# Kernel optimization log

Measured on AMD Instinct MI355X. Metric: run time of the kernel, lower is better.

## Reference

```python
import jax, jax.numpy as jnp
import numpy as np

HD = 64          # head_dim
PX = 32          # patches_x
PY = 32          # patches_y
IW = 512.0       # image_width
IH = 512.0       # image_height
C = 4            # cameras
B = 1
H = 12
S = C * PX * PY  # 4096


def _rope_coeffs(pos, feat_dim):
    nf = feat_dim // 2
    freqs = 100.0 ** (-jnp.arange(nf, dtype=jnp.float32) / nf)  # freq_base=100, freq_scale=1
    ang = pos[:, None].astype(jnp.float32) * freqs[None, :]
    # broadcast shape (1, seqlen, 1, nf)
    return jnp.cos(ang)[None, :, None, :], jnp.sin(ang)[None, :, None, :]


def _rope(x, cs, inverse=False):
    cos, sin = cs
    h = x.shape[-1] // 2
    xi, yi = x[..., :h], x[..., h:]
    if inverse:
        return jnp.concatenate([cos * xi - sin * yi, sin * xi + cos * yi], -1)
    return jnp.concatenate([cos * xi + sin * yi, -sin * xi + cos * yi], -1)


def _proj(x, M):
    # x: (b, s, n, f), M: (b, c, D, D) per-camera projection applied to D-sized sub-blocks
    b, s, n, f = x.shape
    c, D = M.shape[1], M.shape[-1]
    xr = x.reshape(b, c, s // c, n, f // D, D)
    return jnp.einsum('bcij,bcpnkj->bcpnki', M, xr).reshape(b, s, n, f)


def _invert_SE3(T):
    Rinv = jnp.swapaxes(T[..., :3, :3], -1, -2)
    t = -jnp.einsum('...ij,...j->...i', Rinv, T[..., :3, 3])
    top = jnp.concatenate([Rinv, t[..., None]], -1)            # (..., 3, 4)
    bot = jnp.zeros_like(top[..., :1, :]).at[..., 0, 3].set(1.0)
    return jnp.concatenate([top, bot], -2)


def _lift_K(K):
    out = jnp.zeros(K.shape[:-2] + (4, 4), K.dtype)
    return out.at[..., :3, :3].set(K).at[..., 3, 3].set(1.0)


def _invert_K(K):
    out = jnp.zeros_like(K)
    out = out.at[..., 0, 0].set(1.0 / K[..., 0, 0]).at[..., 1, 1].set(1.0 / K[..., 1, 1])
    out = out.at[..., 0, 2].set(-K[..., 0, 2] / K[..., 0, 0]).at[..., 1, 2].set(-K[..., 1, 2] / K[..., 1, 1])
    return out.at[..., 2, 2].set(1.0)


def setup_inputs() -> dict:
    key = jax.random.key(0)
    kq, kk, kv, kr, kt, kf = jax.random.split(key, 6)
    q = jax.random.normal(kq, (B, S, H, HD), dtype=jnp.float32)
    k = jax.random.normal(kk, (B, S, H, HD), dtype=jnp.float32)
    v = jax.random.normal(kv, (B, S, H, HD), dtype=jnp.float32)
    # proper SE(3) viewmats: random rotations (det +1) + translations
    A = jax.random.normal(kr, (B, C, 3, 3), dtype=jnp.float32)
    Q, _ = jnp.linalg.qr(A)
    Q = Q * jnp.sign(jnp.linalg.det(Q))[..., None, None]  # det(sQ)=s^3 det(Q) for 3x3
    t = jax.random.normal(kt, (B, C, 3, 1), dtype=jnp.float32)
    top = jnp.concatenate([Q, t], -1)
    bot = jnp.tile(jnp.array([0.0, 0.0, 0.0, 1.0], jnp.float32)[None, None, None, :], (B, C, 1, 1))
    viewmats = jnp.concatenate([top, bot], -2)
    # realistic pinhole intrinsics
    f = 400.0 + 200.0 * jax.random.uniform(kf, (B, C, 2), dtype=jnp.float32)
    Ks = jnp.zeros((B, C, 3, 3), jnp.float32)
    Ks = Ks.at[..., 0, 0].set(f[..., 0]).at[..., 1, 1].set(f[..., 1])
    Ks = Ks.at[..., 0, 2].set(IW / 2).at[..., 1, 2].set(IH / 2).at[..., 2, 2].set(1.0)
    return {'q': q, 'k': k, 'v': v, 'viewmats': viewmats, 'Ks': Ks}


def reference(q, k, v, viewmats, Ks):
    # normalize intrinsics to [-0.5, 0.5] image coords
    Ksn = jnp.zeros_like(Ks)
    Ksn = Ksn.at[..., 0, 0].set(Ks[..., 0, 0] / IW).at[..., 1, 1].set(Ks[..., 1, 1] / IH)
    Ksn = Ksn.at[..., 0, 2].set(Ks[..., 0, 2] / IW - 0.5).at[..., 1, 2].set(Ks[..., 1, 2] / IH - 0.5)
    Ksn = Ksn.at[..., 2, 2].set(1.0)
    P = jnp.einsum('...ij,...jk->...ik', _lift_K(Ksn), viewmats)         # (B,C,4,4)
    P_T = jnp.swapaxes(P, -1, -2)
    P_inv = jnp.einsum('...ij,...jk->...ik', _invert_SE3(viewmats), _lift_K(_invert_K(Ksn)))
    # 2-D patch positions, tiled over cameras (num_register_tokens=0)
    pos_x = jnp.tile(jnp.arange(PX), (PY * C,))
    pos_y = jnp.tile(jnp.repeat(jnp.arange(PY), PX), (C,))
    cx = _rope_coeffs(pos_x, HD // 4)
    cy = _rope_coeffs(pos_y, HD // 4)
    h2, h4 = HD // 2, HD // 4

    def tq(x):
        return jnp.concatenate([_proj(x[..., :h2], P_T), _rope(x[..., h2:h2 + h4], cx), _rope(x[..., h2 + h4:], cy)], -1)

    def tkv(x):
        return jnp.concatenate([_proj(x[..., :h2], P_inv), _rope(x[..., h2:h2 + h4], cx), _rope(x[..., h2 + h4:], cy)], -1)

    def to(x):
        return jnp.concatenate([_proj(x[..., :h2], P), _rope(x[..., h2:h2 + h4], cx, True), _rope(x[..., h2 + h4:], cy, True)], -1)

    qh, kh, vh = tq(q), tkv(k), tkv(v)
    scale = 1.0 / jnp.sqrt(jnp.float32(HD))
    scores = jnp.einsum('bqhd,bkhd->bhqk', qh, kh) * scale
    w = jax.nn.softmax(scores, axis=-1)
    out = jnp.einsum('bhqk,bkhd->bqhd', w, vh)
    return to(out)
```

## Files before the change

### kernel.cpp

```cpp
#include <hip/hip_runtime.h>
#include <cstdint>

#define SQ 4096
#define NH 12
#define NC 4
#define KVB 64
#define NSPLIT 4
#define NTS (SQ / NSPLIT / KVB)

typedef __attribute__((ext_vector_type(8))) __bf16 bf16x8;
typedef __attribute__((ext_vector_type(8))) short short8;
typedef __attribute__((ext_vector_type(4))) short s16x4;
typedef __attribute__((ext_vector_type(4))) float f32x4;
typedef __attribute__((ext_vector_type(16))) float f32x16;
typedef __attribute__((ext_vector_type(4))) unsigned int u32x4;
typedef __attribute__((ext_vector_type(2))) unsigned int u32x2;

__device__ __forceinline__ unsigned short f2bf(float f) {
  unsigned int u = __float_as_uint(f);
  u += 0x7FFFu + ((u >> 16) & 1u);
  return (unsigned short)(u >> 16);
}
__device__ __forceinline__ float bf2f(unsigned short u) {
  return __uint_as_float(((unsigned int)u) << 16);
}
__device__ __forceinline__ unsigned int cvtpk(float lo, float hi) {
  unsigned int r;
  asm("v_cvt_pk_bf16_f32 %0, %1, %2" : "=v"(r) : "v"(lo), "v"(hi));
  return r;
}

__device__ __constant__ float FRQ[8] = {
    1.0f, 0.5623413251903491f, 0.31622776601683794f, 0.17782794100389229f,
    0.1f, 0.05623413251903491f, 0.031622776601683794f, 0.017782794100389229f};

__device__ __forceinline__ float4 mat4(const float4 M[4], float4 x) {
  float4 y;
  y.x = M[0].x * x.x + M[0].y * x.y + M[0].z * x.z + M[0].w * x.w;
  y.y = M[1].x * x.x + M[1].y * x.y + M[1].z * x.z + M[1].w * x.w;
  y.z = M[2].x * x.x + M[2].y * x.y + M[2].z * x.z + M[2].w * x.w;
  y.w = M[3].x * x.x + M[3].y * x.y + M[3].z * x.z + M[3].w * x.w;
  return y;
}
__device__ __forceinline__ float4 rope4(float4 x, float4 p, float4 c, float4 sn, float sgn) {
  float4 y;
  y.x = c.x * x.x + sgn * sn.x * p.x;
  y.y = c.y * x.y + sgn * sn.y * p.y;
  y.z = c.z * x.z + sgn * sn.z * p.z;
  y.w = c.w * x.w + sgn * sn.w * p.w;
  return y;
}
__device__ __forceinline__ float4 sxor2(float4 x) {
  float4 p;
  p.x = __shfl_xor(x.x, 2); p.y = __shfl_xor(x.y, 2);
  p.z = __shfl_xor(x.z, 2); p.w = __shfl_xor(x.w, 2);
  return p;
}
__device__ __forceinline__ void store_bf4(unsigned short* p, float4 v) {
  s16x4 r;
  r[0] = (short)f2bf(v.x); r[1] = (short)f2bf(v.y);
  r[2] = (short)f2bf(v.z); r[3] = (short)f2bf(v.w);
  *(s16x4*)p = r;
}

__device__ __forceinline__ void build_tables(const float* __restrict__ viewmats,
                                             const float* __restrict__ Ks,
                                             float* __restrict__ mats,
                                             float* __restrict__ ct, float* __restrict__ st) {
  const int t = threadIdx.x;
  if (t < 256) {
    int pos = t >> 3, jf = t & 7;
    float rev = (float)pos * FRQ[jf] * 0.15915494309189535f;
    ct[t] = __builtin_amdgcn_cosf(rev);
    st[t] = __builtin_amdgcn_sinf(rev);
  }
  if (t < NC) {
    const float* V = viewmats + t * 16;
    const float* K = Ks + t * 9;
    float fx = K[0] * (1.0f / 512.0f);
    float fy = K[4] * (1.0f / 512.0f);
    float cx = K[2] * (1.0f / 512.0f) - 0.5f;
    float cy = K[5] * (1.0f / 512.0f) - 0.5f;
    float P[16], PT[16], IV[16], PI[16];
    for (int jj = 0; jj < 4; jj++) {
      P[0 * 4 + jj] = fx * V[0 * 4 + jj] + cx * V[2 * 4 + jj];
      P[1 * 4 + jj] = fy * V[1 * 4 + jj] + cy * V[2 * 4 + jj];
      P[2 * 4 + jj] = V[2 * 4 + jj];
      P[3 * 4 + jj] = V[3 * 4 + jj];
    }
    for (int i = 0; i < 4; i++)
      for (int jj = 0; jj < 4; jj++) PT[i * 4 + jj] = P[jj * 4 + i];
    for (int i = 0; i < 3; i++) {
      for (int jj = 0; jj < 3; jj++) IV[i * 4 + jj] = V[jj * 4 + i];
      IV[i * 4 + 3] = -(V[3] * V[0 * 4 + i] + V[7] * V[1 * 4 + i] + V[11] * V[2 * 4 + i]);
    }
    IV[12] = 0.f; IV[13] = 0.f; IV[14] = 0.f; IV[15] = 1.f;
    float rfx = 1.0f / fx, rfy = 1.0f / fy;
    for (int i = 0; i < 4; i++) {
      PI[i * 4 + 0] = IV[i * 4 + 0] * rfx;
      PI[i * 4 + 1] = IV[i * 4 + 1] * rfy;
      PI[i * 4 + 2] = -cx * rfx * IV[i * 4 + 0] - cy * rfy * IV[i * 4 + 1] + IV[i * 4 + 2];
      PI[i * 4 + 3] = IV[i * 4 + 3];
    }
    for (int ii = 0; ii < 16; ii++) {
      mats[0   + t * 16 + ii] = PT[ii];
      mats[64  + t * 16 + ii] = PI[ii];
      mats[128 + t * 16 + ii] = P[ii];
    }
  }
}

__global__ __launch_bounds__(256) void transform_kernel(
    const float* __restrict__ q, const float* __restrict__ k, const float* __restrict__ v,
    const float* __restrict__ viewmats, const float* __restrict__ Ks,
    unsigned short* __restrict__ qh, unsigned short* __restrict__ kh, unsigned short* __restrict__ vh) {
  __shared__ float TB[192 + 512];
  float* mats = TB;
  float* CT = TB + 192;
  float* ST = TB + 448;
  build_tables(viewmats, Ks, mats, CT, ST);
  __syncthreads();

  const int t = threadIdx.x;
  const int j = t & 15;
  const int rbase = blockIdx.x * 48;
  const int cam = (rbase / NH) >> 10;

  float4 Mq[4], Mk[4];
  if (j < 8) {
    const float4* mq = (const float4*)(mats + cam * 16);
    const float4* mk = (const float4*)(mats + 64 + cam * 16);
#pragma unroll
    for (int i = 0; i < 4; ++i) { Mq[i] = mq[i]; Mk[i] = mk[i]; }
  }

#pragma unroll
  for (int itr = 0; itr < 3; ++itr) {
    const int row = rbase + itr * 16 + (t >> 4);
    const int s = row / NH;
    const int h = row - s * NH;
    const size_t ioff = (size_t)row * 64 + j * 4;
    const size_t ooff = (size_t)h * (SQ * 64) + (size_t)s * 64 + j * 4;
    float4 xq = *(const float4*)(q + ioff);
    float4 xk = *(const float4*)(k + ioff);
    float4 xv = *(const float4*)(v + ioff);
    float4 pq = sxor2(xq), pk = sxor2(xk), pv = sxor2(xv);
    float4 yq, yk, yv;
    if (j < 8) {
      yq = mat4(Mq, xq); yk = mat4(Mk, xk); yv = mat4(Mk, xv);
    } else {
      bool isx = (((j >> 1) & 1) == 0);
      float sgn = isx ? 1.0f : -1.0f;
      int pos = (j < 12) ? (s & 31) : ((s >> 5) & 31);
      int fb = (j & 1) * 4;
      float4 c = *(const float4*)(CT + pos * 8 + fb);
      float4 sn = *(const float4*)(ST + pos * 8 + fb);
      yq = rope4(xq, pq, c, sn, sgn);
      yk = rope4(xk, pk, c, sn, sgn);
      yv = rope4(xv, pv, c, sn, sgn);
    }
    const float SC = 0.1803368801111204f;
    yq.x *= SC; yq.y *= SC; yq.z *= SC; yq.w *= SC;
    store_bf4(qh + ooff, yq);
    store_bf4(kh + ooff, yk);
    store_bf4(vh + ooff, yv);
  }
}

__global__ __launch_bounds__(128, 3) void attn_kernel(const unsigned short* __restrict__ qh,
                                                      const unsigned short* __restrict__ kh,
                                                      const unsigned short* __restrict__ vh,
                                                      unsigned short* __restrict__ opart,
                                                      float* __restrict__ lbuf) {
  __shared__ __align__(16) short Kl[KVB * 64];
  __shared__ __align__(16) short Vl[KVB * 64];
  const int t = threadIdx.x;
  const int lane = t & 63;
  const int w = t >> 6;
  const int hi = lane >> 5;
  const int l31 = lane & 31;
  const int sw7 = l31 & 7;
  const int h = blockIdx.y;
  const int sp = blockIdx.z;
  const int q0 = blockIdx.x * 64 + w * 32;
  const int kbase = sp * (SQ / NSPLIT);
  const size_t hbase = (size_t)h * SQ * 64;

  bf16x8 qf[4];
  {
    const unsigned short* qp = qh + hbase + (size_t)(q0 + l31) * 64 + hi * 8;
#pragma unroll
    for (int ds = 0; ds < 4; ++ds) qf[ds] = *(const bf16x8*)(qp + ds * 16);
  }

  int kr[4], kg[4], kidx[4];
#pragma unroll
  for (int i = 0; i < 4; ++i) {
    int c = t + 128 * i;
    kr[i] = c >> 3;
    kg[i] = c & 7;
    kidx[i] = kr[i] * 64 + ((kg[i] ^ (kr[i] & 7)) << 3);
  }
  const int va = t & 15;
  const int vD0 = (t >> 4) * 8;

  float l = 0.f;
  f32x16 oac0, oac1;
#pragma unroll
  for (int r = 0; r < 16; ++r) { oac0[r] = 0.f; oac1[r] = 0.f; }

  short8 kst[4], vst[4];

  auto issue_loads = [&](int kt) {
#pragma unroll
    for (int i = 0; i < 4; ++i)
      kst[i] = *(const short8*)(kh + hbase + (size_t)(kt + kr[i]) * 64 + kg[i] * 8);
    const unsigned short* vp = vh + hbase + (size_t)(kt + 4 * va) * 64 + vD0;
#pragma unroll
    for (int i = 0; i < 4; ++i) vst[i] = *(const short8*)(vp + i * 64);
  };

  auto write_lds = [&]() {
#pragma unroll
    for (int i = 0; i < 4; ++i) *(short8*)(Kl + kidx[i]) = kst[i];
#pragma unroll
    for (int dd = 0; dd < 8; ++dd) {
      int d = vD0 + dd;
      unsigned int w0 = (unsigned int)(unsigned short)vst[0][dd] |
                        ((unsigned int)(unsigned short)vst[1][dd] << 16);
      unsigned int w1 = (unsigned int)(unsigned short)vst[2][dd] |
                        ((unsigned int)(unsigned short)vst[3][dd] << 16);
      u32x2 pk; pk[0] = w0; pk[1] = w1;
      int idx = d * 64 + ((((va >> 1)) ^ (d & 7)) << 3) + (va & 1) * 4;
      *(u32x2*)(Vl + idx) = pk;
    }
  };

  issue_loads(kbase);
  write_lds();
  __syncthreads();

#define MKFRAG(sv, base, out)                                          \
  {                                                                    \
    unsigned int a0 = cvtpk(sv[base + 0], sv[base + 1]);               \
    unsigned int b0 = cvtpk(sv[base + 4], sv[base + 5]);               \
    asm volatile("v_permlane32_swap_b32 %0, %1" : "+v"(a0), "+v"(b0)); \
    unsigned int a1 = cvtpk(sv[base + 2], sv[base + 3]);               \
    unsigned int b1 = cvtpk(sv[base + 6], sv[base + 7]);               \
    asm volatile("v_permlane32_swap_b32 %0, %1" : "+v"(a1), "+v"(b1)); \
    u32x4 u; u[0] = a0; u[1] = a1; u[2] = b0; u[3] = b1;               \
    out = __builtin_bit_cast(bf16x8, u);                               \
  }

  for (int it = 0; it < NTS; ++it) {
    const bool pf = (it + 1 < NTS);
    if (pf) issue_loads(kbase + (it + 1) * KVB);

    f32x16 s0, s1;
#pragma unroll
    for (int r = 0; r < 16; ++r) { s0[r] = 0.f; s1[r] = 0.f; }
    __builtin_amdgcn_s_setprio(1);
#pragma unroll
    for (int ds = 0; ds < 4; ++ds) {
      bf16x8 k0 = *(const bf16x8*)(Kl + (0 * 32 + l31) * 64 + (((hi + 2 * ds) ^ sw7) << 3));
      bf16x8 k1 = *(const bf16x8*)(Kl + (1 * 32 + l31) * 64 + (((hi + 2 * ds) ^ sw7) << 3));
      s0 = __builtin_amdgcn_mfma_f32_32x32x16_bf16(k0, qf[ds], s0, 0, 0, 0);
      s1 = __builtin_amdgcn_mfma_f32_32x32x16_bf16(k1, qf[ds], s1, 0, 0, 0);
    }
    __builtin_amdgcn_s_setprio(0);

    float rs = 0.f;
#pragma unroll
    for (int r = 0; r < 16; ++r) { s0[r] = __builtin_amdgcn_exp2f(s0[r]); rs += s0[r]; }
#pragma unroll
    for (int r = 0; r < 16; ++r) { s1[r] = __builtin_amdgcn_exp2f(s1[r]); rs += s1[r]; }
    rs += __shfl_xor(rs, 32);
    l += rs;

    bf16x8 pa00, pa01, pa10, pa11;
    MKFRAG(s0, 0, pa00);
    MKFRAG(s0, 8, pa01);
    MKFRAG(s1, 0, pa10);
    MKFRAG(s1, 8, pa11);

    __builtin_amdgcn_s_setprio(1);
#pragma unroll
    for (int db = 0; db < 2; ++db) {
      const int rb = (db * 32 + l31) * 64;
      bf16x8 v00 = *(const bf16x8*)(Vl + rb + (((0 + hi) ^ sw7) << 3));
      bf16x8 v01 = *(const bf16x8*)(Vl + rb + (((2 + hi) ^ sw7) << 3));
      bf16x8 v10 = *(const bf16x8*)(Vl + rb + (((4 + hi) ^ sw7) << 3));
      bf16x8 v11 = *(const bf16x8*)(Vl + rb + (((6 + hi) ^ sw7) << 3));
      if (db == 0) {
        oac0 = __builtin_amdgcn_mfma_f32_32x32x16_bf16(pa00, v00, oac0, 0, 0, 0);
        oac0 = __builtin_amdgcn_mfma_f32_32x32x16_bf16(pa01, v01, oac0, 0, 0, 0);
        oac0 = __builtin_amdgcn_mfma_f32_32x32x16_bf16(pa10, v10, oac0, 0, 0, 0);
        oac0 = __builtin_amdgcn_mfma_f32_32x32x16_bf16(pa11, v11, oac0, 0, 0, 0);
      } else {
        oac1 = __builtin_amdgcn_mfma_f32_32x32x16_bf16(pa00, v00, oac1, 0, 0, 0);
        oac1 = __builtin_amdgcn_mfma_f32_32x32x16_bf16(pa01, v01, oac1, 0, 0, 0);
        oac1 = __builtin_amdgcn_mfma_f32_32x32x16_bf16(pa10, v10, oac1, 0, 0, 0);
        oac1 = __builtin_amdgcn_mfma_f32_32x32x16_bf16(pa11, v11, oac1, 0, 0, 0);
      }
    }
    __builtin_amdgcn_s_setprio(0);
    __syncthreads();
    if (pf) {
      write_lds();
      __syncthreads();
    }
  }

  float linv = 1.0f / l;
  unsigned short* op = opart + (size_t)sp * NH * SQ * 64 + hbase;
#pragma unroll
  for (int r = 0; r < 16; ++r) {
    int qrow = (r & 3) + 8 * (r >> 2) + 4 * hi;
    float lv = __shfl(linv, qrow);
    op[(size_t)(q0 + qrow) * 64 + l31] = f2bf(oac0[r] * lv);
    op[(size_t)(q0 + qrow) * 64 + 32 + l31] = f2bf(oac1[r] * lv);
  }
  if (hi == 0) lbuf[(size_t)sp * NH * SQ + (size_t)h * SQ + q0 + l31] = l;
}

__global__ __launch_bounds__(256) void outtr_kernel(const unsigned short* __restrict__ opart,
                                                    const float* __restrict__ lbuf,
                                                    const float* __restrict__ viewmats,
                                                    const float* __restrict__ Ks,
                                                    float* __restrict__ out) {
  __shared__ float TB[192 + 512];
  float* mats = TB;
  float* CT = TB + 192;
  float* ST = TB + 448;
  build_tables(viewmats, Ks, mats, CT, ST);
  __syncthreads();

  const int t = threadIdx.x;
  const int j = t & 15;
  const int rbase = blockIdx.x * 48;
  const int cam = (rbase / NH) >> 10;

  float4 M[4];
  if (j < 8) {
    const float4* mp = (const float4*)(mats + 128 + cam * 16);
#pragma unroll
    for (int i = 0; i < 4; ++i) M[i] = mp[i];
  }

#pragma unroll
  for (int itr = 0; itr < 3; ++itr) {
    const int row = rbase + itr * 16 + (t >> 4);
    const int s = row / NH;
    const int h = row - s * NH;

    const size_t HSZ = (size_t)NH * SQ * 64;
    float lv[NSPLIT];
    float lsum = 0.f;
#pragma unroll
    for (int sp = 0; sp < NSPLIT; ++sp) {
      lv[sp] = lbuf[(size_t)sp * NH * SQ + (size_t)h * SQ + s];
      lsum += lv[sp];
    }
    float inv = 1.0f / lsum;

    const size_t po = (size_t)h * (SQ * 64) + (size_t)s * 64 + j * 4;
    float4 x = make_float4(0.f, 0.f, 0.f, 0.f);
#pragma unroll
    for (int sp = 0; sp < NSPLIT; ++sp) {
      s16x4 rr = *(const s16x4*)(opart + (size_t)sp * HSZ + po);
      float wv = lv[sp] * inv;
      x.x += bf2f((unsigned short)rr[0]) * wv;
      x.y += bf2f((unsigned short)rr[1]) * wv;
      x.z += bf2f((unsigned short)rr[2]) * wv;
      x.w += bf2f((unsigned short)rr[3]) * wv;
    }

    float4 p = sxor2(x);
    float4 y;
    if (j < 8) {
      y = mat4(M, x);
    } else {
      bool isx = (((j >> 1) & 1) == 0);
      float sgn = isx ? -1.0f : 1.0f;
      int pos = (j < 12) ? (s & 31) : ((s >> 5) & 31);
      int fb = (j & 1) * 4;
      float4 c = *(const float4*)(CT + pos * 8 + fb);
      float4 sn = *(const float4*)(ST + pos * 8 + fb);
      y = rope4(x, p, c, sn, sgn);
    }
    *(float4*)(out + (size_t)row * 64 + j * 4) = y;
  }
}

extern "C" void kernel_launch(void* const* d_in, const int* in_sizes, int n_in,
                              void* d_out, int out_size, void* d_ws, size_t ws_size,
                              hipStream_t stream) {
  const float* q = (const float*)d_in[0];
  const float* k = (const float*)d_in[1];
  const float* v = (const float*)d_in[2];
  const float* vm = (const float*)d_in[3];
  const float* Ks = (const float*)d_in[4];

  char* ws = (char*)d_ws;
  const size_t HSZ = (size_t)NH * SQ * 64;
  unsigned short* qh = (unsigned short*)(ws + 4096);
  unsigned short* kh = qh + HSZ;
  unsigned short* vh = kh + HSZ;
  unsigned short* opart = vh + HSZ;
  float* lbuf = (float*)(opart + (size_t)NSPLIT * HSZ);

  hipLaunchKernelGGL(transform_kernel, dim3((SQ * NH) / 48), dim3(256), 0, stream,
                     q, k, v, vm, Ks, qh, kh, vh);
  hipLaunchKernelGGL(attn_kernel, dim3(SQ / 64, NH, NSPLIT), dim3(128), 0, stream,
                     qh, kh, vh, opart, lbuf);
  hipLaunchKernelGGL(outtr_kernel, dim3((SQ * NH) / 48), dim3(256), 0, stream,
                     opart, lbuf, vm, Ks, (float*)d_out);
}
```

Before: 178.0 us.

## Halve KV tile to 32, use padded LDS rows, raise occupancy to 4 blocks

```diff
diff --git a/kernel.cpp b/kernel.cpp
--- a/kernel.cpp
+++ b/kernel.cpp
@@ -4,7 +4,7 @@
 #define SQ 4096
 #define NH 12
 #define NC 4
-#define KVB 64
+#define KVB 32
 #define NSPLIT 4
 #define NTS (SQ / NSPLIT / KVB)
 
@@ -14,7 +14,6 @@
 typedef __attribute__((ext_vector_type(4))) float f32x4;
 typedef __attribute__((ext_vector_type(16))) float f32x16;
 typedef __attribute__((ext_vector_type(4))) unsigned int u32x4;
-typedef __attribute__((ext_vector_type(2))) unsigned int u32x2;
 
 __device__ __forceinline__ unsigned short f2bf(float f) {
   unsigned int u = __float_as_uint(f);
@@ -167,19 +166,18 @@
   }
 }
 
-__global__ __launch_bounds__(128, 3) void attn_kernel(const unsigned short* __restrict__ qh,
+__global__ __launch_bounds__(128, 4) void attn_kernel(const unsigned short* __restrict__ qh,
                                                       const unsigned short* __restrict__ kh,
                                                       const unsigned short* __restrict__ vh,
                                                       unsigned short* __restrict__ opart,
                                                       float* __restrict__ lbuf) {
-  __shared__ __align__(16) short Kl[KVB * 64];
-  __shared__ __align__(16) short Vl[KVB * 64];
+  __shared__ __align__(16) short Kl[KVB * 72];
+  __shared__ __align__(16) short Vl[64 * 72];
   const int t = threadIdx.x;
   const int lane = t & 63;
   const int w = t >> 6;
   const int hi = lane >> 5;
   const int l31 = lane & 31;
-  const int sw7 = l31 & 7;
   const int h = blockIdx.y;
   const int sp = blockIdx.z;
   const int q0 = blockIdx.x * 64 + w * 32;
@@ -193,46 +191,32 @@
     for (int ds = 0; ds < 4; ++ds) qf[ds] = *(const bf16x8*)(qp + ds * 16);
   }
 
-  int kr[4], kg[4], kidx[4];
-#pragma unroll
-  for (int i = 0; i < 4; ++i) {
-    int c = t + 128 * i;
-    kr[i] = c >> 3;
-    kg[i] = c & 7;
-    kidx[i] = kr[i] * 64 + ((kg[i] ^ (kr[i] & 7)) << 3);
-  }
-  const int va = t & 15;
-  const int vD0 = (t >> 4) * 8;
+  const int kr0 = t >> 3, kg0 = t & 7;
+  const int kr1 = (t + 128) >> 3, kg1 = t & 7;
+  const int kp = t & 15, dg = t >> 4;
 
   float l = 0.f;
   f32x16 oac0, oac1;
 #pragma unroll
   for (int r = 0; r < 16; ++r) { oac0[r] = 0.f; oac1[r] = 0.f; }
 
-  short8 kst[4], vst[4];
+  short8 kst0, kst1, vst0, vst1;
 
   auto issue_loads = [&](int kt) {
-#pragma unroll
-    for (int i = 0; i < 4; ++i)
-      kst[i] = *(const short8*)(kh + hbase + (size_t)(kt + kr[i]) * 64 + kg[i] * 8);
-    const unsigned short* vp = vh + hbase + (size_t)(kt + 4 * va) * 64 + vD0;
-#pragma unroll
-    for (int i = 0; i < 4; ++i) vst[i] = *(const short8*)(vp + i * 64);
+    kst0 = *(const short8*)(kh + hbase + (size_t)(kt + kr0) * 64 + kg0 * 8);
+    kst1 = *(const short8*)(kh + hbase + (size_t)(kt + kr1) * 64 + kg1 * 8);
+    vst0 = *(const short8*)(vh + hbase + (size_t)(kt + 2 * kp) * 64 + dg * 8);
+    vst1 = *(const short8*)(vh + hbase + (size_t)(kt + 2 * kp + 1) * 64 + dg * 8);
   };
 
   auto write_lds = [&]() {
-#pragma unroll
-    for (int i = 0; i < 4; ++i) *(short8*)(Kl + kidx[i]) = kst[i];
+    *(short8*)(Kl + kr0 * 72 + kg0 * 8) = kst0;
+    *(short8*)(Kl + kr1 * 72 + kg1 * 8) = kst1;
 #pragma unroll
     for (int dd = 0; dd < 8; ++dd) {
-      int d = vD0 + dd;
-      unsigned int w0 = (unsigned int)(unsigned short)vst[0][dd] |
-                        ((unsigned int)(unsigned short)vst[1][dd] << 16);
-      unsigned int w1 = (unsigned int)(unsigned short)vst[2][dd] |
-                        ((unsigned int)(unsigned short)vst[3][dd] << 16);
-      u32x2 pk; pk[0] = w0; pk[1] = w1;
-      int idx = d * 64 + ((((va >> 1)) ^ (d & 7)) << 3) + (va & 1) * 4;
-      *(u32x2*)(Vl + idx) = pk;
+      unsigned int wv = (unsigned int)(unsigned short)vst0[dd] |
+                        ((unsigned int)(unsigned short)vst1[dd] << 16);
+      *(unsigned int*)(Vl + (dg * 8 + dd) * 72 + 2 * kp) = wv;
     }
   };
 
@@ -256,52 +240,39 @@
     const bool pf = (it + 1 < NTS);
     if (pf) issue_loads(kbase + (it + 1) * KVB);
 
-    f32x16 s0, s1;
-#pragma unroll
-    for (int r = 0; r < 16; ++r) { s0[r] = 0.f; s1[r] = 0.f; }
+    f32x16 s;
+#pragma unroll
+    for (int r = 0; r < 16; ++r) s[r] = 0.f;
     __builtin_amdgcn_s_setprio(1);
 #pragma unroll
     for (int ds = 0; ds < 4; ++ds) {
-      bf16x8 k0 = *(const bf16x8*)(Kl + (0 * 32 + l31) * 64 + (((hi + 2 * ds) ^ sw7) << 3));
-      bf16x8 k1 = *(const bf16x8*)(Kl + (1 * 32 + l31) * 64 + (((hi + 2 * ds) ^ sw7) << 3));
-      s0 = __builtin_amdgcn_mfma_f32_32x32x16_bf16(k0, qf[ds], s0, 0, 0, 0);
-      s1 = __builtin_amdgcn_mfma_f32_32x32x16_bf16(k1, qf[ds], s1, 0, 0, 0);
+      bf16x8 kf = *(const bf16x8*)(Kl + l31 * 72 + ((2 * ds + hi) << 3));
+      s = __builtin_amdgcn_mfma_f32_32x32x16_bf16(kf, qf[ds], s, 0, 0, 0);
     }
     __builtin_amdgcn_s_setprio(0);
 
     float rs = 0.f;
 #pragma unroll
-    for (int r = 0; r < 16; ++r) { s0[r] = __builtin_amdgcn_exp2f(s0[r]); rs += s0[r]; }
-#pragma unroll
-    for (int r = 0; r < 16; ++r) { s1[r] = __builtin_amdgcn_exp2f(s1[r]); rs += s1[r]; }
+    for (int r = 0; r < 16; ++r) { s[r] = __builtin_amdgcn_exp2f(s[r]); rs += s[r]; }
     rs += __shfl_xor(rs, 32);
     l += rs;
 
-    bf16x8 pa00, pa01, pa10, pa11;
-    MKFRAG(s0, 0, pa00);
-    MKFRAG(s0, 8, pa01);
-    MKFRAG(s1, 0, pa10);
-    MKFRAG(s1, 8, pa11);
+    bf16x8 paA, paB;
+    MKFRAG(s, 0, paA);
+    MKFRAG(s, 8, paB);
 
     __builtin_amdgcn_s_setprio(1);
-#pragma unroll
-    for (int db = 0; db < 2; ++db) {
-      const int rb = (db * 32 + l31) * 64;
-      bf16x8 v00 = *(const bf16x8*)(Vl + rb + (((0 + hi) ^ sw7) << 3));
-      bf16x8 v01 = *(const bf16x8*)(Vl + rb + (((2 + hi) ^ sw7) << 3));
-      bf16x8 v10 = *(const bf16x8*)(Vl + rb + (((4 + hi) ^ sw7) << 3));
-      bf16x8 v11 = *(const bf16x8*)(Vl + rb + (((6 + hi) ^ sw7) << 3));
-      if (db == 0) {
-        oac0 = __builtin_amdgcn_mfma_f32_32x32x16_bf16(pa00, v00, oac0, 0, 0, 0);
-        oac0 = __builtin_amdgcn_mfma_f32_32x32x16_bf16(pa01, v01, oac0, 0, 0, 0);
-        oac0 = __builtin_amdgcn_mfma_f32_32x32x16_bf16(pa10, v10, oac0, 0, 0, 0);
-        oac0 = __builtin_amdgcn_mfma_f32_32x32x16_bf16(pa11, v11, oac0, 0, 0, 0);
-      } else {
-        oac1 = __builtin_amdgcn_mfma_f32_32x32x16_bf16(pa00, v00, oac1, 0, 0, 0);
-        oac1 = __builtin_amdgcn_mfma_f32_32x32x16_bf16(pa01, v01, oac1, 0, 0, 0);
-        oac1 = __builtin_amdgcn_mfma_f32_32x32x16_bf16(pa10, v10, oac1, 0, 0, 0);
-        oac1 = __builtin_amdgcn_mfma_f32_32x32x16_bf16(pa11, v11, oac1, 0, 0, 0);
-      }
+    {
+      const short* Vr0 = Vl + l31 * 72;
+      const short* Vr1 = Vl + (32 + l31) * 72;
+      bf16x8 va0 = *(const bf16x8*)(Vr0 + (hi << 3));
+      bf16x8 vb0 = *(const bf16x8*)(Vr0 + ((2 + hi) << 3));
+      bf16x8 va1 = *(const bf16x8*)(Vr1 + (hi << 3));
+      bf16x8 vb1 = *(const bf16x8*)(Vr1 + ((2 + hi) << 3));
+      oac0 = __builtin_amdgcn_mfma_f32_32x32x16_bf16(paA, va0, oac0, 0, 0, 0);
+      oac0 = __builtin_amdgcn_mfma_f32_32x32x16_bf16(paB, vb0, oac0, 0, 0, 0);
+      oac1 = __builtin_amdgcn_mfma_f32_32x32x16_bf16(paA, va1, oac1, 0, 0, 0);
+      oac1 = __builtin_amdgcn_mfma_f32_32x32x16_bf16(paB, vb1, oac1, 0, 0, 0);
     }
     __builtin_amdgcn_s_setprio(0);
     __syncthreads();
```

New measurement: 177.1 us. Within noise of the previous version (-0.5%).
